# Performance work log

Measured on AMD Instinct MI355X. Metric: run time of the kernel, lower is better.

## Reference

```python
import jax, jax.numpy as jnp
import numpy as np

N_HEADS = 4
D_K = 32
C = 128
SCALE = D_K ** (-0.5)


def setup_inputs() -> dict:
    key = jax.random.key(0)
    k1, k2, k3, k4, k5 = jax.random.split(key, 5)
    x = jax.random.normal(k1, (16, C, 32, 32), dtype=jnp.float32)
    # nn.Linear(C, n_heads*d_k*3): weight [out, in], bias [out]
    Wp = jax.random.normal(k2, (N_HEADS * D_K * 3, C), dtype=jnp.float32) * (C ** -0.5)
    bp = jax.random.normal(k3, (N_HEADS * D_K * 3,), dtype=jnp.float32) * 0.01
    # nn.Linear(n_heads*d_k, C)
    Wo = jax.random.normal(k4, (C, N_HEADS * D_K), dtype=jnp.float32) * ((N_HEADS * D_K) ** -0.5)
    bo = jax.random.normal(k5, (C,), dtype=jnp.float32) * 0.01
    return {"x": x, "Wp": Wp, "bp": bp, "Wo": Wo, "bo": bo}


def reference(x, Wp, bp, Wo, bo):
    b, c, h, w = x.shape
    n = h * w
    # (b,c,h,w) -> (b, n, c); NOTE: GroupNorm from __init__ is never applied in forward.
    xf = x.reshape(b, c, n).transpose(0, 2, 1)
    qkv = (xf @ Wp.T + bp).reshape(b, n, N_HEADS, 3 * D_K)
    q, k, v = jnp.split(qkv, 3, axis=-1)  # each (b, n, heads, d_k)
    attn = jnp.einsum('bihd,bjhd->bijh', q, k) * SCALE  # (b, n, n, heads)
    # Faithful to original: softmax over LAST axis = heads axis (original code bug)
    attn = jax.nn.softmax(attn, axis=-1)
    res = jnp.einsum('bijh,bjhd->bihd', attn, v).reshape(b, n, N_HEADS * D_K)
    res = res @ Wo.T + bo + xf
    return res.transpose(0, 2, 1).reshape(b, c, h, w)
```

## Files before the change

kernel.cpp:

```cpp
#include <hip/hip_runtime.h>

typedef short s8v __attribute__((ext_vector_type(8)));
typedef float f4v __attribute__((ext_vector_type(4)));

#define NTOK 1024
#define CD 128
#define QSCALE 0.25506953149031838f

__device__ __forceinline__ ushort f2bf(float x) {
    union { float f; unsigned u; } v; v.f = x;
    unsigned u = v.u + 0x7fff + ((v.u >> 16) & 1);
    return (ushort)(u >> 16);
}
__device__ __forceinline__ float bf2f(ushort x) {
    union { unsigned u; float f; } v; v.u = ((unsigned)x) << 16;
    return v.f;
}
__device__ __forceinline__ void gl_lds16(const ushort* g, ushort* l) {
    __builtin_amdgcn_global_load_lds(
        (const __attribute__((address_space(1))) unsigned int*)(g),
        (__attribute__((address_space(3))) unsigned int*)(l), 16, 0, 0);
}
__device__ __forceinline__ unsigned cvt_pk_bf16(float lo, float hi) {
    unsigned r;
    asm("v_cvt_pk_bf16_f32 %0, %1, %2" : "=v"(r) : "v"(lo), "v"(hi));
    return r;
}

__global__ __launch_bounds__(256) void k_pre(const float* __restrict__ x,
                                             const float* __restrict__ Wp,
                                             const float* __restrict__ Wo,
                                             ushort* __restrict__ xt,
                                             ushort* __restrict__ wpre) {
    const int t = threadIdx.x;
    const int bx = blockIdx.x;
    if (bx < 256) {
        __shared__ ushort tile[128 * 68];
        const int b = bx >> 4;
        const int n0 = (bx & 15) << 6;
        #pragma unroll
        for (int p = 0; p < 8; ++p) {
            const int c = p * 16 + (t >> 4);
            const int n4 = t & 15;
            const float4 v = *(const float4*)&x[(b * CD + c) * NTOK + n0 + n4 * 4];
            ushort4 o;
            o.x = f2bf(v.x); o.y = f2bf(v.y); o.z = f2bf(v.z); o.w = f2bf(v.w);
            *(ushort4*)&tile[c * 68 + n4 * 4] = o;
        }
        __syncthreads();
        #pragma unroll
        for (int p = 0; p < 4; ++p) {
            const int nl = t >> 2;
            const int g = (t & 3) + p * 4;
            s8v tmp;
            #pragma unroll
            for (int e = 0; e < 8; ++e) tmp[e] = (short)tile[(g * 8 + e) * 68 + nl];
            const int n = n0 + nl;
            *(s8v*)&xt[(b * NTOK + n) * CD + ((g ^ (nl & 7)) * 8)] = tmp;
        }
    } else {
        const int kind = bx - 256;
        ushort* dst = wpre + kind * (CD * CD);
        for (int e = t * 4; e < CD * CD; e += 1024) {
            const int f = e >> 7, c = e & 127;
            const float* src;
            if (kind == 3) src = &Wo[f * CD + c];
            else           src = &Wp[((f >> 5) * 96 + kind * 32 + (f & 31)) * CD + c];
            const float4 v = *(const float4*)src;
            ushort4 o;
            o.x = f2bf(v.x); o.y = f2bf(v.y); o.z = f2bf(v.z); o.w = f2bf(v.w);
            *(ushort4*)&dst[f * CD + (((c >> 3) ^ (f & 7)) * 8) + (c & 7)] = o;
        }
    }
}

__global__ __launch_bounds__(256) void k_proj(const ushort* __restrict__ xt,
                                              const ushort* __restrict__ wpre,
                                              const float* __restrict__ bp,
                                              ushort* __restrict__ qb,
                                              ushort* __restrict__ kb,
                                              ushort* __restrict__ vtb) {
    __shared__ ushort Abuf[128 * 128];
    __shared__ ushort Bbuf[64 * 128];
    const int t = threadIdx.x;
    const int lane = t & 63;
    const int w = t >> 6;
    const int li = lane & 15;
    const int lg = lane >> 4;
    const int bx = blockIdx.x;
    const int kind = bx >> 8;
    const int idx = bx & 255;

    const ushort* Asrc;
    const ushort* Bsrc;
    if (kind < 2) {
        Asrc = xt + (idx >> 1) * 128 * CD;
        Bsrc = wpre + kind * (CD * CD) + (idx & 1) * 64 * CD;
    } else {
        Asrc = wpre + 2 * (CD * CD);
        Bsrc = xt + idx * 64 * CD;
    }
    {
        const ushort* ga = Asrc + w * 4096;
        ushort* la = Abuf + w * 4096;
        #pragma unroll
        for (int i = 0; i < 8; ++i) gl_lds16(ga + i * 512 + lane * 8, la + i * 512);
        const ushort* gb = Bsrc + w * 2048;
        ushort* lb = Bbuf + w * 2048;
        #pragma unroll
        for (int i = 0; i < 4; ++i) gl_lds16(gb + i * 512 + lane * 8, lb + i * 512);
    }
    __syncthreads();

    const f4v fz = {0.f, 0.f, 0.f, 0.f};
    f4v acc[2][4];
    #pragma unroll
    for (int mf = 0; mf < 2; ++mf)
        #pragma unroll
        for (int nf = 0; nf < 4; ++nf) acc[mf][nf] = fz;
    const int m_base = w * 32;
    #pragma unroll
    for (int kk = 0; kk < 4; ++kk) {
        s8v a[2], bb[4];
        #pragma unroll
        for (int mf = 0; mf < 2; ++mf) {
            const int row = m_base + mf * 16 + li;
            a[mf] = *(const s8v*)&Abuf[row * CD + (((kk * 4 + lg) ^ (row & 7)) * 8)];
        }
        #pragma unroll
        for (int nf = 0; nf < 4; ++nf) {
            const int row = nf * 16 + li;
            bb[nf] = *(const s8v*)&Bbuf[row * CD + (((kk * 4 + lg) ^ (row & 7)) * 8)];
        }
        #pragma unroll
        for (int mf = 0; mf < 2; ++mf)
            #pragma unroll
            for (int nf = 0; nf < 4; ++nf)
                acc[mf][nf] = __builtin_amdgcn_mfma_f32_16x16x32_bf16(a[mf], bb[nf], acc[mf][nf], 0, 0, 0);
    }

    if (kind < 2) {
        ushort* dst = (kind == 0) ? qb : kb;
        const int m0 = (idx >> 1) * 128;
        const int f0 = (idx & 1) * 64;
        #pragma unroll
        for (int mf = 0; mf < 2; ++mf)
            #pragma unroll
            for (int nf = 0; nf < 4; ++nf) {
                const int f = f0 + nf * 16 + li;
                const int o = (f >> 5) * 96 + kind * 32 + (f & 31);
                const float bias = bp[o];
                #pragma unroll
                for (int r = 0; r < 4; ++r) {
                    const int row = m0 + m_base + mf * 16 + lg * 4 + r;
                    float v = acc[mf][nf][r] + bias;
                    if (kind == 0) v *= QSCALE;
                    dst[row * CD + f] = f2bf(v);
                }
            }
    } else {
        const int n0g = idx * 64;
        const int b = n0g >> 10;
        const int nl0 = n0g & 1023;
        #pragma unroll
        for (int mf = 0; mf < 2; ++mf)
            #pragma unroll
            for (int r = 0; r < 4; ++r) {
                const int f = m_base + mf * 16 + lg * 4 + r;
                const int o = (f >> 5) * 96 + 64 + (f & 31);
                const float bias = bp[o];
                #pragma unroll
                for (int nf = 0; nf < 4; ++nf) {
                    const int n = nl0 + nf * 16 + li;
                    const int jl = n & 31;
                    const int np = (n & ~31) | (((jl & 15) >> 2) * 8 + (jl & 3) + ((jl >> 4) << 2));
                    vtb[(b * CD + f) * NTOK + np] = f2bf(acc[mf][nf][r] + bias);
                }
            }
    }
}

__global__ __launch_bounds__(256) void k_attn(const ushort* __restrict__ qb,
                                              const ushort* __restrict__ kb,
                                              const ushort* __restrict__ vtb,
                                              ushort* __restrict__ res4) {
    __shared__ ushort kbuf[2][32 * 128];
    __shared__ ushort vbuf[2][128 * 40];
    const int t = threadIdx.x;
    const int lane = t & 63;
    const int w = t >> 6;
    const int b = blockIdx.x;
    const int it = blockIdx.y;
    const int js = blockIdx.z;
    const int i0 = it * 64 + w * 16;
    const int li = lane & 15;
    const int lg = lane >> 4;

    s8v qf[4];
    #pragma unroll
    for (int h = 0; h < 4; ++h)
        qf[h] = *(const s8v*)&qb[(b*NTOK + i0 + li)*CD + h*32 + lg*8];

    const f4v fz = {0.f, 0.f, 0.f, 0.f};
    f4v acc[4][2];
    #pragma unroll
    for (int h = 0; h < 4; ++h) { acc[h][0] = fz; acc[h][1] = fz; }

    const int j0 = js * 256;
    const int kr0 = (w*2)*4 + (lane>>4);
    const int kr1 = (w*2+1)*4 + (lane>>4);
    const ushort* ksrc0 = &kb[(b*NTOK + j0 + kr0)*CD + (((lane&15) ^ (kr0&7))*8)];
    const ushort* ksrc1 = &kb[(b*NTOK + j0 + kr1)*CD + (((lane&15) ^ (kr1&7))*8)];
    const ushort* vptr0 = &vtb[(b*CD + (t>>2))*NTOK + j0 + (t&3)*8];
    const ushort* vptr1 = vptr0 + 64*NTOK;
    const int vwo = (t>>2)*40 + (t&3)*8;

    gl_lds16(ksrc0, &kbuf[0][w*1024]);
    gl_lds16(ksrc1, &kbuf[0][w*1024 + 512]);
    s8v v0 = *(const s8v*)vptr0;
    s8v v1 = *(const s8v*)vptr1;
    *(s8v*)&vbuf[0][vwo]          = v0;
    *(s8v*)&vbuf[0][vwo + 64*40]  = v1;
    gl_lds16(ksrc0 + 32*CD, &kbuf[1][w*1024]);
    gl_lds16(ksrc1 + 32*CD, &kbuf[1][w*1024 + 512]);
    v0 = *(const s8v*)(vptr0 + 32);
    v1 = *(const s8v*)(vptr1 + 32);
    __syncthreads();

    unsigned wv[4][4];
    {
        f4v sv[4][2];
        #pragma unroll
        for (int h = 0; h < 4; ++h)
            #pragma unroll
            for (int jh = 0; jh < 2; ++jh) {
                const int row = jh*16 + li;
                s8v kf = *(const s8v*)&kbuf[0][row*128 + (((h*4 + lg) ^ (li & 7))*8)];
                sv[h][jh] = __builtin_amdgcn_mfma_f32_16x16x32_bf16(kf, qf[h], fz, 0, 0, 0);
            }
        #pragma unroll
        for (int jh = 0; jh < 2; ++jh)
            #pragma unroll
            for (int r = 0; r < 4; ++r) {
                float e0 = __builtin_amdgcn_exp2f(sv[0][jh][r]);
                float e1 = __builtin_amdgcn_exp2f(sv[1][jh][r]);
                float e2 = __builtin_amdgcn_exp2f(sv[2][jh][r]);
                float e3 = __builtin_amdgcn_exp2f(sv[3][jh][r]);
                float inv = __builtin_amdgcn_rcpf(e0 + e1 + e2 + e3);
                sv[0][jh][r] = e0 * inv;
                sv[1][jh][r] = e1 * inv;
                sv[2][jh][r] = e2 * inv;
                sv[3][jh][r] = e3 * inv;
            }
        #pragma unroll
        for (int h = 0; h < 4; ++h) {
            wv[h][0] = cvt_pk_bf16(sv[h][0][0], sv[h][0][1]);
            wv[h][1] = cvt_pk_bf16(sv[h][0][2], sv[h][0][3]);
            wv[h][2] = cvt_pk_bf16(sv[h][1][0], sv[h][1][1]);
            wv[h][3] = cvt_pk_bf16(sv[h][1][2], sv[h][1][3]);
        }
    }

    #pragma unroll
    for (int tt = 1; tt <= 8; ++tt) {
        __syncthreads();
        if (tt <= 7) {
            ushort* vn = vbuf[tt & 1];
            *(s8v*)&vn[vwo]          = v0;
            *(s8v*)&vn[vwo + 64*40]  = v1;
        }
        if (tt <= 6) {
            gl_lds16(ksrc0 + (tt+1)*32*CD, &kbuf[(tt+1) & 1][w*1024]);
            gl_lds16(ksrc1 + (tt+1)*32*CD, &kbuf[(tt+1) & 1][w*1024 + 512]);
        }
        if (tt <= 6) {
            v0 = *(const s8v*)(vptr0 + (tt+1)*32);
            v1 = *(const s8v*)(vptr1 + (tt+1)*32);
        }
        f4v sv[4][2];
        if (tt <= 7) {
            const ushort* kc = kbuf[tt & 1];
            #pragma unroll
            for (int h = 0; h < 4; ++h)
                #pragma unroll
                for (int jh = 0; jh < 2; ++jh) {
                    const int row = jh*16 + li;
                    s8v kf = *(const s8v*)&kc[row*128 + (((h*4 + lg) ^ (li & 7))*8)];
                    sv[h][jh] = __builtin_amdgcn_mfma_f32_16x16x32_bf16(kf, qf[h], fz, 0, 0, 0);
                }
        }
        {
            const ushort* vc = vbuf[(tt - 1) & 1];
            #pragma unroll
            for (int h = 0; h < 4; ++h) {
                union { unsigned d[4]; s8v s; } av;
                av.d[0] = wv[h][0]; av.d[1] = wv[h][1];
                av.d[2] = wv[h][2]; av.d[3] = wv[h][3];
                s8v vf0 = *(const s8v*)&vc[(h*32 + li)*40 + lg*8];
                s8v vf1 = *(const s8v*)&vc[(h*32 + 16 + li)*40 + lg*8];
                acc[h][0] = __builtin_amdgcn_mfma_f32_16x16x32_bf16(av.s, vf0, acc[h][0], 0, 0, 0);
                acc[h][1] = __builtin_amdgcn_mfma_f32_16x16x32_bf16(av.s, vf1, acc[h][1], 0, 0, 0);
            }
        }
        if (tt <= 7) {
            #pragma unroll
            for (int jh = 0; jh < 2; ++jh)
                #pragma unroll
                for (int r = 0; r < 4; ++r) {
                    float e0 = __builtin_amdgcn_exp2f(sv[0][jh][r]);
                    float e1 = __builtin_amdgcn_exp2f(sv[1][jh][r]);
                    float e2 = __builtin_amdgcn_exp2f(sv[2][jh][r]);
                    float e3 = __builtin_amdgcn_exp2f(sv[3][jh][r]);
                    float inv = __builtin_amdgcn_rcpf(e0 + e1 + e2 + e3);
                    sv[0][jh][r] = e0 * inv;
                    sv[1][jh][r] = e1 * inv;
                    sv[2][jh][r] = e2 * inv;
                    sv[3][jh][r] = e3 * inv;
                }
            #pragma unroll
            for (int h = 0; h < 4; ++h) {
                wv[h][0] = cvt_pk_bf16(sv[h][0][0], sv[h][0][1]);
                wv[h][1] = cvt_pk_bf16(sv[h][0][2], sv[h][0][3]);
                wv[h][2] = cvt_pk_bf16(sv[h][1][0], sv[h][1][1]);
                wv[h][3] = cvt_pk_bf16(sv[h][1][2], sv[h][1][3]);
            }
        }
    }

    #pragma unroll
    for (int h = 0; h < 4; ++h)
        #pragma unroll
        for (int dh = 0; dh < 2; ++dh)
            #pragma unroll
            for (int r = 0; r < 4; ++r) {
                const int i = i0 + lg*4 + r;
                const int f = h*32 + dh*16 + li;
                res4[js*(16*NTOK*CD) + (b*NTOK + i)*CD + f] = f2bf(acc[h][dh][r]);
            }
}

__global__ __launch_bounds__(256) void k_out(const ushort* __restrict__ wpre,
                                             const ushort* __restrict__ res4,
                                             const float* __restrict__ bo,
                                             const float* __restrict__ x,
                                             float* __restrict__ out) {
    __shared__ ushort Abuf[128 * 128];
    __shared__ ushort Bbuf[64 * 128];
    const int t = threadIdx.x;
    const int lane = t & 63;
    const int w = t >> 6;
    const int li = lane & 15;
    const int lg = lane >> 4;
    const int idx = blockIdx.x;
    const int n0g = idx * 64;
    const int b = n0g >> 10;
    {
        const ushort* ga = wpre + 3 * (CD * CD) + w * 4096;
        ushort* la = Abuf + w * 4096;
        #pragma unroll
        for (int i = 0; i < 8; ++i) gl_lds16(ga + i * 512 + lane * 8, la + i * 512);
    }
    for (int u = t; u < 64 * 16; u += 256) {
        const int rl = u >> 4, g = u & 15;
        const ushort* p = &res4[(n0g + rl) * CD + g * 8];
        s8v p0 = *(const s8v*)(p);
        s8v p1 = *(const s8v*)(p + 16*NTOK*CD);
        s8v p2 = *(const s8v*)(p + 32*NTOK*CD);
        s8v p3 = *(const s8v*)(p + 48*NTOK*CD);
        s8v sm;
        #pragma unroll
        for (int e = 0; e < 8; ++e)
            sm[e] = (short)f2bf(bf2f((ushort)p0[e]) + bf2f((ushort)p1[e])
                              + bf2f((ushort)p2[e]) + bf2f((ushort)p3[e]));
        *(s8v*)&Bbuf[rl * CD + ((g ^ (rl & 7)) * 8)] = sm;
    }
    __syncthreads();

    const f4v fz = {0.f, 0.f, 0.f, 0.f};
    f4v acc[2][4];
    #pragma unroll
    for (int mf = 0; mf < 2; ++mf)
        #pragma unroll
        for (int nf = 0; nf < 4; ++nf) acc[mf][nf] = fz;
    const int m_base = w * 32;
    #pragma unroll
    for (int kk = 0; kk < 4; ++kk) {
        s8v a[2], bb[4];
        #pragma unroll
        for (int mf = 0; mf < 2; ++mf) {
            const int row = m_base + mf * 16 + li;
            a[mf] = *(const s8v*)&Abuf[row * CD + (((kk * 4 + lg) ^ (row & 7)) * 8)];
        }
        #pragma unroll
        for (int nf = 0; nf < 4; ++nf) {
            const int row = nf * 16 + li;
            bb[nf] = *(const s8v*)&Bbuf[row * CD + (((kk * 4 + lg) ^ (row & 7)) * 8)];
        }
        #pragma unroll
        for (int mf = 0; mf < 2; ++mf)
            #pragma unroll
            for (int nf = 0; nf < 4; ++nf)
                acc[mf][nf] = __builtin_amdgcn_mfma_f32_16x16x32_bf16(a[mf], bb[nf], acc[mf][nf], 0, 0, 0);
    }
    const int nl0 = n0g & 1023;
    #pragma unroll
    for (int mf = 0; mf < 2; ++mf)
        #pragma unroll
        for (int r = 0; r < 4; ++r) {
            const int o = m_base + mf * 16 + lg * 4 + r;
            const float bias = bo[o];
            #pragma unroll
            for (int nf = 0; nf < 4; ++nf) {
                const int n = nl0 + nf * 16 + li;
                const int gi = (b * CD + o) * NTOK + n;
                out[gi] = acc[mf][nf][r] + bias + x[gi];
            }
        }
}

extern "C" void kernel_launch(void* const* d_in, const int* in_sizes, int n_in,
                              void* d_out, int out_size, void* d_ws, size_t ws_size,
                              hipStream_t stream) {
    const float* x  = (const float*)d_in[0];
    const float* Wp = (const float*)d_in[1];
    const float* bp = (const float*)d_in[2];
    const float* Wo = (const float*)d_in[3];
    const float* bo = (const float*)d_in[4];
    float* out = (float*)d_out;
    ushort* xt   = (ushort*)d_ws;
    ushort* wpre = xt + 16*1024*128;
    ushort* qbw  = wpre + 4*128*128;
    ushort* kbw  = qbw + 16*1024*128;
    ushort* vtb  = kbw + 16*1024*128;
    ushort* res4 = vtb + 16*1024*128;
    k_pre <<<260, 256, 0, stream>>>(x, Wp, Wo, xt, wpre);
    k_proj<<<768, 256, 0, stream>>>(xt, wpre, bp, qbw, kbw, vtb);
    k_attn<<<dim3(16, 16, 4), 256, 0, stream>>>(qbw, kbw, vtb, res4);
    k_out <<<256, 256, 0, stream>>>(wpre, res4, bo, x, out);
}
```

Before: 49.08 us.

## Process two query row-tiles per wave in attention to reuse K/V loads

Each wave in k_attn now handles 32 query rows (two 16-row MFMA tiles) instead of 16, so every K fragment and V fragment read from LDS feeds twice as many MFMAs. The grid's y dimension is halved, which also halves the total global/LDS staging of K and V across blocks. The cost is higher register pressure (double the accumulators, Q fragments and softmax weights) and half as many blocks (512), which may reduce occupancy and latency hiding.

```diff
diff --git a/kernel.cpp b/kernel.cpp
--- a/kernel.cpp
+++ b/kernel.cpp
@@ -192,19 +192,25 @@
     const int b = blockIdx.x;
     const int it = blockIdx.y;
     const int js = blockIdx.z;
-    const int i0 = it * 64 + w * 16;
+    const int i0 = it * 128 + w * 32;
     const int li = lane & 15;
     const int lg = lane >> 4;
 
-    s8v qf[4];
+    s8v qf[4][2];
     #pragma unroll
     for (int h = 0; h < 4; ++h)
-        qf[h] = *(const s8v*)&qb[(b*NTOK + i0 + li)*CD + h*32 + lg*8];
+        #pragma unroll
+        for (int im = 0; im < 2; ++im)
+            qf[h][im] = *(const s8v*)&qb[(b*NTOK + i0 + im*16 + li)*CD + h*32 + lg*8];
 
     const f4v fz = {0.f, 0.f, 0.f, 0.f};
-    f4v acc[4][2];
-    #pragma unroll
-    for (int h = 0; h < 4; ++h) { acc[h][0] = fz; acc[h][1] = fz; }
+    f4v acc[4][2][2];
+    #pragma unroll
+    for (int h = 0; h < 4; ++h)
+        #pragma unroll
+        for (int dh = 0; dh < 2; ++dh)
+            #pragma unroll
+            for (int im = 0; im < 2; ++im) acc[h][dh][im] = fz;
 
     const int j0 = js * 256;
     const int kr0 = (w*2)*4 + (lane>>4);
@@ -227,82 +233,24 @@
     v1 = *(const s8v*)(vptr1 + 32);
     __syncthreads();
 
-    unsigned wv[4][4];
+    unsigned wv[2][4][4];
     {
-        f4v sv[4][2];
+        s8v kf[4][2];
         #pragma unroll
         for (int h = 0; h < 4; ++h)
             #pragma unroll
             for (int jh = 0; jh < 2; ++jh) {
                 const int row = jh*16 + li;
-                s8v kf = *(const s8v*)&kbuf[0][row*128 + (((h*4 + lg) ^ (li & 7))*8)];
-                sv[h][jh] = __builtin_amdgcn_mfma_f32_16x16x32_bf16(kf, qf[h], fz, 0, 0, 0);
-            }
-        #pragma unroll
-        for (int jh = 0; jh < 2; ++jh)
-            #pragma unroll
-            for (int r = 0; r < 4; ++r) {
-                float e0 = __builtin_amdgcn_exp2f(sv[0][jh][r]);
-                float e1 = __builtin_amdgcn_exp2f(sv[1][jh][r]);
-                float e2 = __builtin_amdgcn_exp2f(sv[2][jh][r]);
-                float e3 = __builtin_amdgcn_exp2f(sv[3][jh][r]);
-                float inv = __builtin_amdgcn_rcpf(e0 + e1 + e2 + e3);
-                sv[0][jh][r] = e0 * inv;
-                sv[1][jh][r] = e1 * inv;
-                sv[2][jh][r] = e2 * inv;
-                sv[3][jh][r] = e3 * inv;
-            }
-        #pragma unroll
-        for (int h = 0; h < 4; ++h) {
-            wv[h][0] = cvt_pk_bf16(sv[h][0][0], sv[h][0][1]);
-            wv[h][1] = cvt_pk_bf16(sv[h][0][2], sv[h][0][3]);
-            wv[h][2] = cvt_pk_bf16(sv[h][1][0], sv[h][1][1]);
-            wv[h][3] = cvt_pk_bf16(sv[h][1][2], sv[h][1][3]);
-        }
-    }
-
-    #pragma unroll
-    for (int tt = 1; tt <= 8; ++tt) {
-        __syncthreads();
-        if (tt <= 7) {
-            ushort* vn = vbuf[tt & 1];
-            *(s8v*)&vn[vwo]          = v0;
-            *(s8v*)&vn[vwo + 64*40]  = v1;
-        }
-        if (tt <= 6) {
-            gl_lds16(ksrc0 + (tt+1)*32*CD, &kbuf[(tt+1) & 1][w*1024]);
-            gl_lds16(ksrc1 + (tt+1)*32*CD, &kbuf[(tt+1) & 1][w*1024 + 512]);
-        }
-        if (tt <= 6) {
-            v0 = *(const s8v*)(vptr0 + (tt+1)*32);
-            v1 = *(const s8v*)(vptr1 + (tt+1)*32);
-        }
-        f4v sv[4][2];
-        if (tt <= 7) {
-            const ushort* kc = kbuf[tt & 1];
+                kf[h][jh] = *(const s8v*)&kbuf[0][row*128 + (((h*4 + lg) ^ (li & 7))*8)];
+            }
+        #pragma unroll
+        for (int im = 0; im < 2; ++im) {
+            f4v sv[4][2];
             #pragma unroll
             for (int h = 0; h < 4; ++h)
                 #pragma unroll
-                for (int jh = 0; jh < 2; ++jh) {
-                    const int row = jh*16 + li;
-                    s8v kf = *(const s8v*)&kc[row*128 + (((h*4 + lg) ^ (li & 7))*8)];
-                    sv[h][jh] = __builtin_amdgcn_mfma_f32_16x16x32_bf16(kf, qf[h], fz, 0, 0, 0);
-                }
-        }
-        {
-            const ushort* vc = vbuf[(tt - 1) & 1];
-            #pragma unroll
-            for (int h = 0; h < 4; ++h) {
-                union { unsigned d[4]; s8v s; } av;
-                av.d[0] = wv[h][0]; av.d[1] = wv[h][1];
-                av.d[2] = wv[h][2]; av.d[3] = wv[h][3];
-                s8v vf0 = *(const s8v*)&vc[(h*32 + li)*40 + lg*8];
-                s8v vf1 = *(const s8v*)&vc[(h*32 + 16 + li)*40 + lg*8];
-                acc[h][0] = __builtin_amdgcn_mfma_f32_16x16x32_bf16(av.s, vf0, acc[h][0], 0, 0, 0);
-                acc[h][1] = __builtin_amdgcn_mfma_f32_16x16x32_bf16(av.s, vf1, acc[h][1], 0, 0, 0);
-            }
-        }
-        if (tt <= 7) {
+                for (int jh = 0; jh < 2; ++jh)
+                    sv[h][jh] = __builtin_amdgcn_mfma_f32_16x16x32_bf16(kf[h][jh], qf[h][im], fz, 0, 0, 0);
             #pragma unroll
             for (int jh = 0; jh < 2; ++jh)
                 #pragma unroll
@@ -319,24 +267,104 @@
                 }
             #pragma unroll
             for (int h = 0; h < 4; ++h) {
-                wv[h][0] = cvt_pk_bf16(sv[h][0][0], sv[h][0][1]);
-                wv[h][1] = cvt_pk_bf16(sv[h][0][2], sv[h][0][3]);
-                wv[h][2] = cvt_pk_bf16(sv[h][1][0], sv[h][1][1]);
-                wv[h][3] = cvt_pk_bf16(sv[h][1][2], sv[h][1][3]);
-            }
-        }
-    }
-
-    #pragma unroll
-    for (int h = 0; h < 4; ++h)
-        #pragma unroll
-        for (int dh = 0; dh < 2; ++dh)
-            #pragma unroll
-            for (int r = 0; r < 4; ++r) {
-                const int i = i0 + lg*4 + r;
-                const int f = h*32 + dh*16 + li;
-                res4[js*(16*NTOK*CD) + (b*NTOK + i)*CD + f] = f2bf(acc[h][dh][r]);
-            }
+                wv[im][h][0] = cvt_pk_bf16(sv[h][0][0], sv[h][0][1]);
+                wv[im][h][1] = cvt_pk_bf16(sv[h][0][2], sv[h][0][3]);
+                wv[im][h][2] = cvt_pk_bf16(sv[h][1][0], sv[h][1][1]);
+                wv[im][h][3] = cvt_pk_bf16(sv[h][1][2], sv[h][1][3]);
+            }
+        }
+    }
+
+    #pragma unroll
+    for (int tt = 1; tt <= 8; ++tt) {
+        __syncthreads();
+        if (tt <= 7) {
+            ushort* vn = vbuf[tt & 1];
+            *(s8v*)&vn[vwo]          = v0;
+            *(s8v*)&vn[vwo + 64*40]  = v1;
+        }
+        if (tt <= 6) {
+            gl_lds16(ksrc0 + (tt+1)*32*CD, &kbuf[(tt+1) & 1][w*1024]);
+            gl_lds16(ksrc1 + (tt+1)*32*CD, &kbuf[(tt+1) & 1][w*1024 + 512]);
+        }
+        if (tt <= 6) {
+            v0 = *(const s8v*)(vptr0 + (tt+1)*32);
+            v1 = *(const s8v*)(vptr1 + (tt+1)*32);
+        }
+        s8v kf[4][2];
+        if (tt <= 7) {
+            const ushort* kc = kbuf[tt & 1];
+            #pragma unroll
+            for (int h = 0; h < 4; ++h)
+                #pragma unroll
+                for (int jh = 0; jh < 2; ++jh) {
+                    const int row = jh*16 + li;
+                    kf[h][jh] = *(const s8v*)&kc[row*128 + (((h*4 + lg) ^ (li & 7))*8)];
+                }
+        }
+        {
+            const ushort* vc = vbuf[(tt - 1) & 1];
+            #pragma unroll
+            for (int h = 0; h < 4; ++h) {
+                s8v vf0 = *(const s8v*)&vc[(h*32 + li)*40 + lg*8];
+                s8v vf1 = *(const s8v*)&vc[(h*32 + 16 + li)*40 + lg*8];
+                union { unsigned d[4]; s8v s; } a0, a1;
+                a0.d[0] = wv[0][h][0]; a0.d[1] = wv[0][h][1];
+                a0.d[2] = wv[0][h][2]; a0.d[3] = wv[0][h][3];
+                a1.d[0] = wv[1][h][0]; a1.d[1] = wv[1][h][1];
+                a1.d[2] = wv[1][h][2]; a1.d[3] = wv[1][h][3];
+                acc[h][0][0] = __builtin_amdgcn_mfma_f32_16x16x32_bf16(a0.s, vf0, acc[h][0][0], 0, 0, 0);
+                acc[h][1][0] = __builtin_amdgcn_mfma_f32_16x16x32_bf16(a0.s, vf1, acc[h][1][0], 0, 0, 0);
+                acc[h][0][1] = __builtin_amdgcn_mfma_f32_16x16x32_bf16(a1.s, vf0, acc[h][0][1], 0, 0, 0);
+                acc[h][1][1] = __builtin_amdgcn_mfma_f32_16x16x32_bf16(a1.s, vf1, acc[h][1][1], 0, 0, 0);
+            }
+        }
+        if (tt <= 7) {
+            #pragma unroll
+            for (int im = 0; im < 2; ++im) {
+                f4v sv[4][2];
+                #pragma unroll
+                for (int h = 0; h < 4; ++h)
+                    #pragma unroll
+                    for (int jh = 0; jh < 2; ++jh)
+                        sv[h][jh] = __builtin_amdgcn_mfma_f32_16x16x32_bf16(kf[h][jh], qf[h][im], fz, 0, 0, 0);
+                #pragma unroll
+                for (int jh = 0; jh < 2; ++jh)
+                    #pragma unroll
+                    for (int r = 0; r < 4; ++r) {
+                        float e0 = __builtin_amdgcn_exp2f(sv[0][jh][r]);
+                        float e1 = __builtin_amdgcn_exp2f(sv[1][jh][r]);
+                        float e2 = __builtin_amdgcn_exp2f(sv[2][jh][r]);
+                        float e3 = __builtin_amdgcn_exp2f(sv[3][jh][r]);
+                        float inv = __builtin_amdgcn_rcpf(e0 + e1 + e2 + e3);
+                        sv[0][jh][r] = e0 * inv;
+                        sv[1][jh][r] = e1 * inv;
+                        sv[2][jh][r] = e2 * inv;
+                        sv[3][jh][r] = e3 * inv;
+                    }
+                #pragma unroll
+                for (int h = 0; h < 4; ++h) {
+                    wv[im][h][0] = cvt_pk_bf16(sv[h][0][0], sv[h][0][1]);
+                    wv[im][h][1] = cvt_pk_bf16(sv[h][0][2], sv[h][0][3]);
+                    wv[im][h][2] = cvt_pk_bf16(sv[h][1][0], sv[h][1][1]);
+                    wv[im][h][3] = cvt_pk_bf16(sv[h][1][2], sv[h][1][3]);
+                }
+            }
+        }
+    }
+
+    #pragma unroll
+    for (int im = 0; im < 2; ++im)
+        #pragma unroll
+        for (int h = 0; h < 4; ++h)
+            #pragma unroll
+            for (int dh = 0; dh < 2; ++dh)
+                #pragma unroll
+                for (int r = 0; r < 4; ++r) {
+                    const int i = i0 + im*16 + lg*4 + r;
+                    const int f = h*32 + dh*16 + li;
+                    res4[js*(16*NTOK*CD) + (b*NTOK + i)*CD + f] = f2bf(acc[h][dh][im][r]);
+                }
 }
 
 __global__ __launch_bounds__(256) void k_out(const ushort* __restrict__ wpre,
@@ -435,6 +463,6 @@
     ushort* res4 = vtb + 16*1024*128;
     k_pre <<<260, 256, 0, stream>>>(x, Wp, Wo, xt, wpre);
     k_proj<<<768, 256, 0, stream>>>(xt, wpre, bp, qbw, kbw, vtb);
-    k_attn<<<dim3(16, 16, 4), 256, 0, stream>>>(qbw, kbw, vtb, res4);
+    k_attn<<<dim3(16, 8, 4), 256, 0, stream>>>(qbw, kbw, vtb, res4);
     k_out <<<256, 256, 0, stream>>>(wpre, res4, bo, x, out);
 }
```

After: 49.67 us. No clear change (+1.2%).
